# Kernel tuning notes

Measured on AMD Instinct MI355X. Metric: run time of the kernel, lower is better.

The kernel has to match this reference:

```python
import jax, jax.numpy as jnp
import numpy as np

N = 12288       # tree nodes
V = 1000        # wordpiece vocab (len(char_list))
EMBDIM = 256    # embdim
EMBSIZE = 32    # embsize (GCN hidden)


def setup_inputs() -> dict:
    key = jax.random.key(0)
    k1, k2, k3, k4 = jax.random.split(key, 4)
    node_ids = jax.random.randint(k1, (N,), 0, V)

    # Build a random prefix-tree topology: parent[i] < i for i >= 1.
    rng = np.random.default_rng(0)
    parents = (rng.random(N - 1) * np.arange(1, N)).astype(np.int64)
    children = np.arange(1, N, dtype=np.int64)
    self_loops = np.stack([np.arange(N, dtype=np.int64)] * 2, axis=1)   # [N,2]
    pc = np.stack([parents, children], axis=1)                           # [N-1,2]
    edges = jnp.asarray(np.concatenate([self_loops, pc], axis=0))        # [2N-1,2]

    embed_table = jax.random.normal(k2, (V, EMBDIM), dtype=jnp.float32) * 0.02
    W1 = jax.random.normal(k3, (EMBDIM, EMBSIZE), dtype=jnp.float32) / np.sqrt(EMBDIM)
    b1 = jnp.zeros((EMBSIZE,), dtype=jnp.float32)
    W2 = jax.random.normal(k4, (EMBSIZE, EMBSIZE), dtype=jnp.float32) / np.sqrt(EMBSIZE)
    b2 = jnp.zeros((EMBSIZE,), dtype=jnp.float32)
    return {"node_ids": node_ids, "edges": edges, "embed_table": embed_table,
            "W1": W1, "b1": b1, "W2": W2, "b2": b2}


def reference(node_ids, edges, embed_table, W1, b1, W2, b2):
    # Embedding gather for every tree node (dropout is identity at eval).
    emb = embed_table[node_ids]                                   # [N, EMBDIM]
    # Dense adjacency from edge list: self-loops + parent->child (directed).
    A = jnp.zeros((N, N), dtype=embed_table.dtype)
    A = A.at[edges[:, 0], edges[:, 1]].set(1.0)
    # Symmetric degree normalization D^{-1/2} A D^{-1/2} (degrees = row sums).
    d = jnp.sum(A, axis=-1) ** -0.5                               # rows have >=1 (self-loop)
    A_norm = d[:, None] * A * d[None, :]
    # Two-layer GCN.
    h = jax.nn.relu(A_norm @ (emb @ W1 + b1))                     # [N, EMBSIZE]
    h = jax.nn.relu(A_norm @ (h @ W2 + b2))                       # [N, EMBSIZE]
    return h
```

## Files before the change

kernel.cpp:

```cpp
#include <hip/hip_runtime.h>
#include <hip/hip_bf16.h>

#define NN 12288
#define ED 256
#define ES 32
#define NPC (NN - 1)
#define BLK 256

typedef __hip_bfloat16 bf16;
typedef __attribute__((ext_vector_type(8))) unsigned short u8v;

__device__ __forceinline__ bool detect_f32(const void* W1) {
    const unsigned short* p = (const unsigned short*)W1 + (threadIdx.x & 63) * 8;
    u8v v = *(const u8v*)p;
    int huge = 0;
#pragma unroll
    for (int i = 0; i < 8; ++i) {
        unsigned short m = (unsigned short)(v[i] & 0x7fff);
        huge |= (m >= 0x4620);
    }
    return __any(huge) != 0;
}

__device__ __forceinline__ float ldv(const void* p, int i, bool f32) {
    return f32 ? ((const float*)p)[i] : __bfloat162float(((const bf16*)p)[i]);
}

__global__ __launch_bounds__(BLK)
void k1(const int* __restrict__ node_ids, const int* __restrict__ edges,
        const void* __restrict__ table, const void* __restrict__ W1,
        const void* __restrict__ b1, unsigned* __restrict__ deg,
        float* __restrict__ X) {
    bool f32 = detect_f32(W1);
    unsigned t = blockIdx.x * BLK + threadIdx.x;
    if (t < NPC) atomicAdd(&deg[edges[2 * (NN + t)]], 1u);
    int n = t >> 5, j = t & 31;
    size_t id = (size_t)node_ids[n];
    float acc = ldv(b1, j, f32);
    if (f32) {
        const float* e = (const float*)table + id * ED;
        const float* w = (const float*)W1;
        #pragma unroll 8
        for (int k = 0; k < ED; ++k) acc += e[k] * w[k * ES + j];
    } else {
        const bf16* e = (const bf16*)table + id * ED;
        const bf16* w = (const bf16*)W1;
        #pragma unroll 8
        for (int k = 0; k < ED; ++k)
            acc += __bfloat162float(e[k]) * __bfloat162float(w[k * ES + j]);
    }
    X[t] = acc;
}

__global__ __launch_bounds__(BLK)
void k2(const int* __restrict__ edges, const unsigned* __restrict__ deg,
        const float* __restrict__ X, float* __restrict__ acc1) {
    unsigned t = blockIdx.x * BLK + threadIdx.x;
    if (t >= (unsigned)NPC * ES) return;
    int e = t >> 5, k = t & 31;
    int c = e + 1;
    int r = edges[2 * (NN + e)];
    float w = rsqrtf((float)deg[r] + 1.f) * rsqrtf((float)deg[c] + 1.f);
    atomicAdd(&acc1[r * ES + k], w * X[c * ES + k]);
}

__global__ __launch_bounds__(BLK)
void k3(const int* __restrict__ edges, const void* __restrict__ W1,
        const void* __restrict__ W2, const void* __restrict__ b2,
        const unsigned* __restrict__ deg, const float* __restrict__ acc1,
        const float* __restrict__ X, float* __restrict__ acc2) {
    __shared__ float sW2[ES * 33];
    __shared__ float sB[ES];
    bool f32 = detect_f32(W1);
    int tt = threadIdx.x;
    for (int i = tt; i < ES * ES; i += BLK) sW2[(i >> 5) * 33 + (i & 31)] = ldv(W2, i, f32);
    if (tt < ES) sB[tt] = ldv(b2, tt, f32);
    __syncthreads();
    unsigned t = blockIdx.x * BLK + tt;
    if (t >= (unsigned)NPC * ES) return;
    int e = t >> 5, j = t & 31;
    int c = e + 1;
    int r = edges[2 * (NN + e)];
    float rc = rsqrtf((float)deg[c] + 1.f);
    float h = fmaxf(acc1[c * ES + j] + (rc * rc) * X[c * ES + j], 0.f);
    float x2 = sB[j];
    #pragma unroll
    for (int k = 0; k < ES; ++k)
        x2 += __shfl(h, k, ES) * sW2[k * 33 + j];
    float w = rsqrtf((float)deg[r] + 1.f) * rc;
    atomicAdd(&acc2[r * ES + j], w * x2);
}

__global__ __launch_bounds__(BLK)
void k4(const void* __restrict__ W1, const void* __restrict__ W2,
        const void* __restrict__ b2, const unsigned* __restrict__ deg,
        const float* __restrict__ acc1, const float* __restrict__ X,
        const float* __restrict__ acc2, void* __restrict__ out) {
    __shared__ float sW2[ES * 33];
    __shared__ float sB[ES];
    bool f32 = detect_f32(W1);
    int tt = threadIdx.x;
    for (int i = tt; i < ES * ES; i += BLK) sW2[(i >> 5) * 33 + (i & 31)] = ldv(W2, i, f32);
    if (tt < ES) sB[tt] = ldv(b2, tt, f32);
    __syncthreads();
    unsigned t = blockIdx.x * BLK + tt;
    int n = t >> 5, j = t & 31;
    float rn = rsqrtf((float)deg[n] + 1.f);
    float sw = rn * rn;
    float h = fmaxf(acc1[n * ES + j] + sw * X[n * ES + j], 0.f);
    float x2 = sB[j];
    #pragma unroll
    for (int k = 0; k < ES; ++k)
        x2 += __shfl(h, k, ES) * sW2[k * 33 + j];
    float v = fmaxf(acc2[n * ES + j] + sw * x2, 0.f);
    if (f32) ((float*)out)[t] = v;
    else     ((bf16*)out)[t]  = __float2bfloat16(v);
}

extern "C" void kernel_launch(void* const* d_in, const int* in_sizes, int n_in,
                              void* d_out, int out_size, void* d_ws, size_t ws_size,
                              hipStream_t stream) {
    const int* node_ids = (const int*)d_in[0];
    const int* edges    = (const int*)d_in[1];
    const void* table   = d_in[2];
    const void* W1      = d_in[3];
    const void* b1      = d_in[4];
    const void* W2      = d_in[5];
    const void* b2      = d_in[6];

    char* ws = (char*)d_ws;
    unsigned* deg = (unsigned*)ws;
    float* acc1   = (float*)(ws + (size_t)NN * 4);
    float* acc2   = acc1 + (size_t)NN * ES;
    float* X      = acc2 + (size_t)NN * ES;

    hipMemsetAsync(d_ws, 0, (size_t)NN * 4 + 2ull * NN * ES * 4, stream);

    const int g_node = NN * ES / BLK;
    const int g_edge = (NPC * ES + BLK - 1) / BLK;

    k1<<<g_node, BLK, 0, stream>>>(node_ids, edges, table, W1, b1, deg, X);
    k2<<<g_edge, BLK, 0, stream>>>(edges, deg, X, acc1);
    k3<<<g_edge, BLK, 0, stream>>>(edges, W1, W2, b2, deg, acc1, X, acc2);
    k4<<<g_node, BLK, 0, stream>>>(W1, W2, b2, deg, acc1, X, acc2, d_out);
}
```

Baseline: 107.9 us.

## Compute embedding projection with bf16 MFMA using swizzled transposed W1 in LDS

The first kernel's per-thread 256-long scalar dot product is replaced by 16x16x32 bf16 MFMA tiles, each wave handling 16 nodes. W1 is transposed into LDS as bf16 with an XOR swizzle to avoid bank conflicts, and the grid shrinks to 64 nodes per block. fp32 inputs are rounded to bf16 before the matrix multiply, which reduces precision against the fp32 reference. Each block now also pays for staging W1 into LDS.

New measurement: 88.30 us. 1.22x faster.

```diff
diff --git a/kernel.cpp b/kernel.cpp
--- a/kernel.cpp
+++ b/kernel.cpp
@@ -8,7 +8,9 @@
 #define BLK 256
 
 typedef __hip_bfloat16 bf16;
+typedef __attribute__((ext_vector_type(8))) short s8v;
 typedef __attribute__((ext_vector_type(8))) unsigned short u8v;
+typedef __attribute__((ext_vector_type(4))) float f4v;
 
 __device__ __forceinline__ bool detect_f32(const void* W1) {
     const unsigned short* p = (const unsigned short*)W1 + (threadIdx.x & 63) * 8;
@@ -26,30 +28,82 @@
     return f32 ? ((const float*)p)[i] : __bfloat162float(((const bf16*)p)[i]);
 }
 
+__device__ __forceinline__ unsigned short f2bf(float f) {
+    bf16 h = __float2bfloat16(f);
+    return __builtin_bit_cast(unsigned short, h);
+}
+
 __global__ __launch_bounds__(BLK)
 void k1(const int* __restrict__ node_ids, const int* __restrict__ edges,
         const void* __restrict__ table, const void* __restrict__ W1,
         const void* __restrict__ b1, unsigned* __restrict__ deg,
         float* __restrict__ X) {
+    __shared__ unsigned short sW1T[ES * ED];
     bool f32 = detect_f32(W1);
-    unsigned t = blockIdx.x * BLK + threadIdx.x;
+    int tt = threadIdx.x;
+    unsigned t = blockIdx.x * BLK + tt;
     if (t < NPC) atomicAdd(&deg[edges[2 * (NN + t)]], 1u);
-    int n = t >> 5, j = t & 31;
-    size_t id = (size_t)node_ids[n];
-    float acc = ldv(b1, j, f32);
+
+    {
+        int j = tt & 31, kc = tt >> 5;
+        for (int it = 0; it < 4; ++it) {
+            int kb = kc + 8 * it;
+            u8v v;
+            if (f32) {
+                const float* w = (const float*)W1;
+#pragma unroll
+                for (int e = 0; e < 8; ++e) v[e] = f2bf(w[(kb * 8 + e) * ES + j]);
+            } else {
+                const unsigned short* w = (const unsigned short*)W1;
+#pragma unroll
+                for (int e = 0; e < 8; ++e) v[e] = w[(kb * 8 + e) * ES + j];
+            }
+            *(u8v*)&sW1T[j * ED + ((kb ^ (j & 7)) * 8)] = v;
+        }
+    }
+    __syncthreads();
+
+    int lane = tt & 63;
+    int q = lane & 15, hi = lane >> 4;
+    int n0 = blockIdx.x * 64 + (tt >> 6) * 16;
+    size_t id = (size_t)node_ids[n0 + q];
+    f4v a0 = {0.f, 0.f, 0.f, 0.f}, a1 = {0.f, 0.f, 0.f, 0.f};
+    int sw = q & 7;
     if (f32) {
-        const float* e = (const float*)table + id * ED;
-        const float* w = (const float*)W1;
-        #pragma unroll 8
-        for (int k = 0; k < ED; ++k) acc += e[k] * w[k * ES + j];
+        const float* e = (const float*)table + id * ED + hi * 8;
+#pragma unroll
+        for (int s = 0; s < 8; ++s) {
+            f4v e0 = *(const f4v*)(e + s * 32);
+            f4v e1 = *(const f4v*)(e + s * 32 + 4);
+            u8v av;
+#pragma unroll
+            for (int i = 0; i < 4; ++i) { av[i] = f2bf(e0[i]); av[4 + i] = f2bf(e1[i]); }
+            int blk = (hi + 4 * s) ^ sw;
+            s8v b0  = *(const s8v*)&sW1T[q * ED + blk * 8];
+            s8v b1v = *(const s8v*)&sW1T[(q + 16) * ED + blk * 8];
+            s8v a = __builtin_bit_cast(s8v, av);
+            a0 = __builtin_amdgcn_mfma_f32_16x16x32_bf16(a, b0,  a0, 0, 0, 0);
+            a1 = __builtin_amdgcn_mfma_f32_16x16x32_bf16(a, b1v, a1, 0, 0, 0);
+        }
     } else {
-        const bf16* e = (const bf16*)table + id * ED;
-        const bf16* w = (const bf16*)W1;
-        #pragma unroll 8
-        for (int k = 0; k < ED; ++k)
-            acc += __bfloat162float(e[k]) * __bfloat162float(w[k * ES + j]);
-    }
-    X[t] = acc;
+        const short* e = (const short*)table + id * ED + hi * 8;
+#pragma unroll
+        for (int s = 0; s < 8; ++s) {
+            s8v a = *(const s8v*)(e + s * 32);
+            int blk = (hi + 4 * s) ^ sw;
+            s8v b0  = *(const s8v*)&sW1T[q * ED + blk * 8];
+            s8v b1v = *(const s8v*)&sW1T[(q + 16) * ED + blk * 8];
+            a0 = __builtin_amdgcn_mfma_f32_16x16x32_bf16(a, b0,  a0, 0, 0, 0);
+            a1 = __builtin_amdgcn_mfma_f32_16x16x32_bf16(a, b1v, a1, 0, 0, 0);
+        }
+    }
+    float bv0 = ldv(b1, q, f32), bv1 = ldv(b1, q + 16, f32);
+#pragma unroll
+    for (int i = 0; i < 4; ++i) {
+        int n = n0 + hi * 4 + i;
+        X[n * ES + q]      = a0[i] + bv0;
+        X[n * ES + q + 16] = a1[i] + bv1;
+    }
 }
 
 __global__ __launch_bounds__(BLK)
@@ -136,10 +190,11 @@
 
     hipMemsetAsync(d_ws, 0, (size_t)NN * 4 + 2ull * NN * ES * 4, stream);
 
+    const int g_mfma = NN / 64;
     const int g_node = NN * ES / BLK;
     const int g_edge = (NPC * ES + BLK - 1) / BLK;
 
-    k1<<<g_node, BLK, 0, stream>>>(node_ids, edges, table, W1, b1, deg, X);
+    k1<<<g_mfma, BLK, 0, stream>>>(node_ids, edges, table, W1, b1, deg, X);
     k2<<<g_edge, BLK, 0, stream>>>(edges, deg, X, acc1);
     k3<<<g_edge, BLK, 0, stream>>>(edges, W1, W2, b2, deg, acc1, X, acc2);
     k4<<<g_node, BLK, 0, stream>>>(W1, W2, b2, deg, acc1, X, acc2, d_out);
```
